# Performance work log

Measured on AMD Instinct MI355X. Metric: run time of the kernel, lower is better.

The kernel has to match this reference:

```python
import jax, jax.numpy as jnp
import numpy as np

B, N, DIM, H, DH = 4, 2048, 1024, 16, 64  # batch, seq, model dim, heads, head dim


def setup_inputs() -> dict:
    key = jax.random.key(0)
    k1, k2, k3 = jax.random.split(key, 3)
    x = jax.random.normal(k1, (B, N, DIM), dtype=jnp.float32)
    w_qkv = jax.random.normal(k2, (DIM, 3 * H * DH), dtype=jnp.float32) * (DIM ** -0.5)
    w_out = jax.random.normal(k3, (H * DH, DIM), dtype=jnp.float32) * ((H * DH) ** -0.5)
    b_out = jnp.zeros((DIM,), dtype=jnp.float32)
    return {"x": x, "w_qkv": w_qkv, "w_out": w_out, "b_out": b_out}


def reference(x, w_qkv, w_out, b_out):
    scale = DH ** -0.5
    qkv = x @ w_qkv                              # [b, n, 3*h*d]
    q, k, v = jnp.split(qkv, 3, axis=-1)
    # 'b n (h d) -> b h n d'
    def to_heads(t):
        return t.reshape(B, N, H, DH).transpose(0, 2, 1, 3)
    q, k, v = to_heads(q), to_heads(k), to_heads(v)
    dots = jnp.einsum('bhid,bhjd->bhij', q, k) * scale   # [b, h, n, n]
    attn = jax.nn.softmax(dots, axis=-1)
    out = jnp.einsum('bhij,bhjd->bhid', attn, v)          # [b, h, n, d]
    out = out.transpose(0, 2, 1, 3).reshape(B, N, H * DH) # 'b h n d -> b n (h d)'
    return out @ w_out + b_out
```

## Files before the change

kernel.cpp:

```cpp
#include <hip/hip_runtime.h>
#include <stdint.h>

#define B_    4
#define N_    2048
#define DIM_  1024
#define H_    16
#define DH_   64
#define BN_   (B_ * N_)
#define QKVN_ (3 * H_ * DH_)

typedef unsigned short u16;
typedef __attribute__((ext_vector_type(8))) __bf16 bf16x8;
typedef __attribute__((ext_vector_type(8))) short  short8;
typedef __attribute__((ext_vector_type(4))) float  f32x4;
typedef __attribute__((ext_vector_type(4))) u16    u16x4;

__device__ inline u16 f2bf(float f) {
    union { float f; uint32_t u; } v; v.f = f;
    uint32_t r = v.u + 0x7fffu + ((v.u >> 16) & 1u);
    return (u16)(r >> 16);
}
__device__ inline float bf2f(u16 u) {
    union { uint32_t u; float f; } v; v.u = ((uint32_t)u) << 16;
    return v.f;
}

__global__ __launch_bounds__(256) void cast_f32_bf16(const float* __restrict__ in,
                                                     u16* __restrict__ out, int n4) {
    int i = blockIdx.x * blockDim.x + threadIdx.x;
    int stride = gridDim.x * blockDim.x;
    for (; i < n4; i += stride) {
        float4 v = reinterpret_cast<const float4*>(in)[i];
        u16x4 o;
        o.x = f2bf(v.x); o.y = f2bf(v.y); o.z = f2bf(v.z); o.w = f2bf(v.w);
        reinterpret_cast<u16x4*>(out)[i] = o;
    }
}

__global__ __launch_bounds__(256) void transpose_cast(const float* __restrict__ in,
                                                      u16* __restrict__ out, int R, int C) {
    int gid = blockIdx.x * blockDim.x + threadIdx.x;
    int total = C * (R / 4);
    if (gid >= total) return;
    int n  = gid % C;
    int k4 = (gid / C) * 4;
    u16x4 o;
    o.x = f2bf(in[(size_t)(k4 + 0) * C + n]);
    o.y = f2bf(in[(size_t)(k4 + 1) * C + n]);
    o.z = f2bf(in[(size_t)(k4 + 2) * C + n]);
    o.w = f2bf(in[(size_t)(k4 + 3) * C + n]);
    *reinterpret_cast<u16x4*>(&out[(size_t)n * R + k4]) = o;
}

template <bool BF16_OUT>
__global__ __launch_bounds__(256) void gemm_bt(const u16* __restrict__ A,
                                               const u16* __restrict__ BT,
                                               void* __restrict__ Cout,
                                               const float* __restrict__ bias,
                                               int M, int Nn, int K) {
    __shared__ u16 As[128][40];
    __shared__ u16 Bs[128][40];

    const int tid  = threadIdx.x;
    const int m0   = blockIdx.y * 128;
    const int n0   = blockIdx.x * 128;
    const int w    = tid >> 6;
    const int lane = tid & 63;
    const int lr   = lane & 15;
    const int lg   = lane >> 4;
    const int wm   = w >> 1;
    const int wn   = w & 1;

    f32x4 acc[4][4] = {};

    const int sr = tid >> 2;
    const int sc = (tid & 3) * 8;
    const u16* Aptr = A  + (size_t)(m0 + sr) * K + sc;
    const u16* Bptr = BT + (size_t)(n0 + sr) * K + sc;

    for (int kt = 0; kt < K; kt += 32) {
        *reinterpret_cast<short8*>(&As[sr][sc])      = *reinterpret_cast<const short8*>(Aptr + kt);
        *reinterpret_cast<short8*>(&As[sr + 64][sc]) = *reinterpret_cast<const short8*>(Aptr + (size_t)64 * K + kt);
        *reinterpret_cast<short8*>(&Bs[sr][sc])      = *reinterpret_cast<const short8*>(Bptr + kt);
        *reinterpret_cast<short8*>(&Bs[sr + 64][sc]) = *reinterpret_cast<const short8*>(Bptr + (size_t)64 * K + kt);
        __syncthreads();

        bf16x8 af[4], bfr[4];
#pragma unroll
        for (int m = 0; m < 4; m++)
            af[m] = *reinterpret_cast<const bf16x8*>(&As[wm * 64 + m * 16 + lr][lg * 8]);
#pragma unroll
        for (int n = 0; n < 4; n++)
            bfr[n] = *reinterpret_cast<const bf16x8*>(&Bs[wn * 64 + n * 16 + lr][lg * 8]);
#pragma unroll
        for (int m = 0; m < 4; m++)
#pragma unroll
            for (int n = 0; n < 4; n++)
                acc[m][n] = __builtin_amdgcn_mfma_f32_16x16x32_bf16(af[m], bfr[n], acc[m][n], 0, 0, 0);
        __syncthreads();
    }

#pragma unroll
    for (int m = 0; m < 4; m++)
#pragma unroll
        for (int n = 0; n < 4; n++) {
            const int row = m0 + wm * 64 + m * 16 + lg * 4;
            const int col = n0 + wn * 64 + n * 16 + lr;
#pragma unroll
            for (int r = 0; r < 4; r++) {
                if (BF16_OUT) {
                    ((u16*)Cout)[(size_t)(row + r) * Nn + col] = f2bf(acc[m][n][r]);
                } else {
                    ((float*)Cout)[(size_t)(row + r) * Nn + col] = acc[m][n][r] + bias[col];
                }
            }
        }
}

__global__ __launch_bounds__(256) void attn_kernel(const u16* __restrict__ qkv,
                                                   u16* __restrict__ out) {
    __shared__ __align__(16) u16      Ks[2][64][40];
    __shared__ __align__(16) uint32_t VT32[64 * 36];
    __shared__ __align__(16) u16      Ps[4][16][72];

    const int tid  = threadIdx.x;
    const int w    = tid >> 6;
    const int lane = tid & 63;
    const int lr   = lane & 15;
    const int lg   = lane >> 4;

    const int bh = blockIdx.y;
    const int b  = bh >> 4;
    const int h  = bh & 15;
    const int rowbase = b * N_;
    const int q0 = blockIdx.x * 64;
    const int qoff = h * DH_;

    bf16x8 qf[2];
    {
        const int qrow = rowbase + q0 + w * 16 + lr;
#pragma unroll
        for (int ks = 0; ks < 2; ks++) {
            short8 raw = *reinterpret_cast<const short8*>(
                &qkv[(size_t)qrow * QKVN_ + qoff + ks * 32 + lg * 8]);
            const u16* ru = reinterpret_cast<const u16*>(&raw);
            union { u16 u[8]; bf16x8 v; } q;
#pragma unroll
            for (int j = 0; j < 8; j++) q.u[j] = f2bf(bf2f(ru[j]) * 0.125f);
            qf[ks] = q.v;
        }
    }

    float mrun = -3e38f, lrun = 0.f;
    f32x4 acc_o[4] = {};

    const u16* kg = qkv + (size_t)rowbase * QKVN_ + DIM_ + qoff;
    const u16* vg = qkv + (size_t)rowbase * QKVN_ + 2 * DIM_ + qoff;

    const int kr = tid >> 2;
    const int kc = (tid & 3) * 8;
    const size_t koff0 = (size_t)kr * QKVN_ + kc;
    const int vp  = tid >> 3;
    const int vsc = (tid & 7) * 8;
    const size_t voff0 = (size_t)(vp * 2) * QKVN_ + vsc;
    const size_t voff1 = voff0 + QKVN_;

    short8 kst[2], vst[2];
    kst[0] = *reinterpret_cast<const short8*>(kg + koff0);
    kst[1] = *reinterpret_cast<const short8*>(kg + koff0 + 32);
    vst[0] = *reinterpret_cast<const short8*>(vg + voff0);
    vst[1] = *reinterpret_cast<const short8*>(vg + voff1);

    *reinterpret_cast<short8*>(&Ks[0][kr][kc]) = kst[0];
    *reinterpret_cast<short8*>(&Ks[1][kr][kc]) = kst[1];
    {
        const u16* v0 = reinterpret_cast<const u16*>(&vst[0]);
        const u16* v1 = reinterpret_cast<const u16*>(&vst[1]);
#pragma unroll
        for (int i = 0; i < 8; i++) {
            const int d = vsc + i;
            const int col = vp ^ (((d >> 2) & 7) << 2);
            VT32[d * 36 + col] = (uint32_t)v0[i] | ((uint32_t)v1[i] << 16);
        }
    }
    __syncthreads();

    for (int t = 0; t < N_ / 64; t++) {
        if (t + 1 < N_ / 64) {
            const u16* kg2 = kg + (size_t)(t + 1) * 64 * QKVN_;
            const u16* vg2 = vg + (size_t)(t + 1) * 64 * QKVN_;
            kst[0] = *reinterpret_cast<const short8*>(kg2 + koff0);
            kst[1] = *reinterpret_cast<const short8*>(kg2 + koff0 + 32);
            vst[0] = *reinterpret_cast<const short8*>(vg2 + voff0);
            vst[1] = *reinterpret_cast<const short8*>(vg2 + voff1);
        }

        f32x4 s[4];
#pragma unroll
        for (int n = 0; n < 4; n++) {
            bf16x8 k0 = *reinterpret_cast<const bf16x8*>(&Ks[0][n * 16 + lr][lg * 8]);
            bf16x8 k1 = *reinterpret_cast<const bf16x8*>(&Ks[1][n * 16 + lr][lg * 8]);
            f32x4 z = {0.f, 0.f, 0.f, 0.f};
            s[n] = __builtin_amdgcn_mfma_f32_16x16x32_bf16(k0, qf[0], z, 0, 0, 0);
            s[n] = __builtin_amdgcn_mfma_f32_16x16x32_bf16(k1, qf[1], s[n], 0, 0, 0);
        }

        float tmax = fmaxf(fmaxf(s[0][0], s[0][1]), fmaxf(s[0][2], s[0][3]));
#pragma unroll
        for (int n = 1; n < 4; n++)
            tmax = fmaxf(tmax, fmaxf(fmaxf(s[n][0], s[n][1]), fmaxf(s[n][2], s[n][3])));
        tmax = fmaxf(tmax, __shfl_xor(tmax, 16));
        tmax = fmaxf(tmax, __shfl_xor(tmax, 32));
        float mnew = fmaxf(mrun, tmax);
        float fac = __expf(mrun - mnew);
        mrun = mnew;
        float psum = 0.f;
#pragma unroll
        for (int n = 0; n < 4; n++) {
            float p0 = __expf(s[n][0] - mnew);
            float p1 = __expf(s[n][1] - mnew);
            float p2 = __expf(s[n][2] - mnew);
            float p3 = __expf(s[n][3] - mnew);
            psum += (p0 + p1) + (p2 + p3);
            u16x4 pw;
            pw.x = f2bf(p0); pw.y = f2bf(p1); pw.z = f2bf(p2); pw.w = f2bf(p3);
            *reinterpret_cast<u16x4*>(&Ps[w][lr][n * 16 + lg * 4]) = pw;
        }
        psum += __shfl_xor(psum, 16);
        psum += __shfl_xor(psum, 32);
        lrun = lrun * fac + psum;

        float facq[4];
#pragma unroll
        for (int r = 0; r < 4; r++) facq[r] = __shfl(fac, (lane & 48) | (lg * 4 + r));
#pragma unroll
        for (int n = 0; n < 4; n++)
#pragma unroll
            for (int r = 0; r < 4; r++) acc_o[n][r] *= facq[r];

#pragma unroll
        for (int c = 0; c < 2; c++) {
            bf16x8 pa = *reinterpret_cast<const bf16x8*>(&Ps[w][lr][c * 32 + lg * 8]);
#pragma unroll
            for (int n = 0; n < 4; n++) {
                const int d = n * 16 + lr;
                const int bc = (c * 16 + lg * 4) ^ (((d >> 2) & 7) << 2);
                bf16x8 vf = *reinterpret_cast<const bf16x8*>(&VT32[d * 36 + bc]);
                acc_o[n] = __builtin_amdgcn_mfma_f32_16x16x32_bf16(pa, vf, acc_o[n], 0, 0, 0);
            }
        }

        __syncthreads();
        if (t + 1 < N_ / 64) {
            *reinterpret_cast<short8*>(&Ks[0][kr][kc]) = kst[0];
            *reinterpret_cast<short8*>(&Ks[1][kr][kc]) = kst[1];
            const u16* v0 = reinterpret_cast<const u16*>(&vst[0]);
            const u16* v1 = reinterpret_cast<const u16*>(&vst[1]);
#pragma unroll
            for (int i = 0; i < 8; i++) {
                const int d = vsc + i;
                const int col = vp ^ (((d >> 2) & 7) << 2);
                VT32[d * 36 + col] = (uint32_t)v0[i] | ((uint32_t)v1[i] << 16);
            }
        }
        __syncthreads();
    }

    float linv = 1.f / lrun;
    float lq[4];
#pragma unroll
    for (int r = 0; r < 4; r++) lq[r] = __shfl(linv, (lane & 48) | (lg * 4 + r));
#pragma unroll
    for (int n = 0; n < 4; n++)
#pragma unroll
        for (int r = 0; r < 4; r++) {
            const int row = rowbase + q0 + w * 16 + lg * 4 + r;
            const int col = qoff + n * 16 + lr;
            out[(size_t)row * DIM_ + col] = f2bf(acc_o[n][r] * lq[r]);
        }
}

extern "C" void kernel_launch(void* const* d_in, const int* in_sizes, int n_in,
                              void* d_out, int out_size, void* d_ws, size_t ws_size,
                              hipStream_t stream) {
    const float* x     = (const float*)d_in[0];
    const float* w_qkv = (const float*)d_in[1];
    const float* w_out = (const float*)d_in[2];
    const float* b_out = (const float*)d_in[3];
    float* out = (float*)d_out;

    char* ws = (char*)d_ws;
    u16* xbf   = (u16*)(ws);
    u16* wqkvT = (u16*)(ws + 16777216);
    u16* woutT = (u16*)(ws + 23068672);
    u16* qkv   = (u16*)(ws + 25165824);
    u16* attnO = (u16*)(ws + 75497472);

    cast_f32_bf16<<<2048, 256, 0, stream>>>(x, xbf, (BN_ * DIM_) / 4);
    transpose_cast<<<(DIM_ / 4) * QKVN_ / 256, 256, 0, stream>>>(w_qkv, wqkvT, DIM_, QKVN_);
    transpose_cast<<<(DIM_ / 4) * DIM_ / 256, 256, 0, stream>>>(w_out, woutT, DIM_, DIM_);

    gemm_bt<true><<<dim3(QKVN_ / 128, BN_ / 128), 256, 0, stream>>>(
        xbf, wqkvT, qkv, nullptr, BN_, QKVN_, DIM_);

    attn_kernel<<<dim3(N_ / 64, B_ * H_), 256, 0, stream>>>(qkv, attnO);

    gemm_bt<false><<<dim3(DIM_ / 128, BN_ / 128), 256, 0, stream>>>(
        attnO, woutT, out, b_out, BN_, DIM_, DIM_);
}
```

Baseline: 363.3 us.

## Use direct global-to-LDS loads, exp2 softmax with lazy rescale, hardware bf16 convert

The GEMM tile load now uses global_load_lds to write straight into unpadded shared memory, skipping the register round trip. The attention kernel folds log2(e) into the Q scale so it can use exp2f. It skips the running-max rescale of the accumulator unless the new max exceeds the old one by more than a threshold. It also precomputes the swizzled V offsets outside the loop and uses the native bf16 conversion instead of manual rounding. The unpadded LDS layout may add bank conflicts on the fragment reads. The lazy rescale keeps the result exact in principle but lets values grow by up to 2^8 before renormalising.

```diff
diff --git a/kernel.cpp b/kernel.cpp
--- a/kernel.cpp
+++ b/kernel.cpp
@@ -9,6 +9,9 @@
 #define BN_   (B_ * N_)
 #define QKVN_ (3 * H_ * DH_)
 
+#define AS1_ __attribute__((address_space(1)))
+#define AS3_ __attribute__((address_space(3)))
+
 typedef unsigned short u16;
 typedef __attribute__((ext_vector_type(8))) __bf16 bf16x8;
 typedef __attribute__((ext_vector_type(8))) short  short8;
@@ -16,9 +19,7 @@
 typedef __attribute__((ext_vector_type(4))) u16    u16x4;
 
 __device__ inline u16 f2bf(float f) {
-    union { float f; uint32_t u; } v; v.f = f;
-    uint32_t r = v.u + 0x7fffu + ((v.u >> 16) & 1u);
-    return (u16)(r >> 16);
+    union { __bf16 b; u16 u; } v; v.b = (__bf16)f; return v.u;
 }
 __device__ inline float bf2f(u16 u) {
     union { uint32_t u; float f; } v; v.u = ((uint32_t)u) << 16;
@@ -58,8 +59,8 @@
                                                void* __restrict__ Cout,
                                                const float* __restrict__ bias,
                                                int M, int Nn, int K) {
-    __shared__ u16 As[128][40];
-    __shared__ u16 Bs[128][40];
+    __shared__ __align__(16) u16 AsF[128 * 32];
+    __shared__ __align__(16) u16 BsF[128 * 32];
 
     const int tid  = threadIdx.x;
     const int m0   = blockIdx.y * 128;
@@ -77,21 +78,26 @@
     const int sc = (tid & 3) * 8;
     const u16* Aptr = A  + (size_t)(m0 + sr) * K + sc;
     const u16* Bptr = BT + (size_t)(n0 + sr) * K + sc;
+    const int ldsb = w * 512;
 
     for (int kt = 0; kt < K; kt += 32) {
-        *reinterpret_cast<short8*>(&As[sr][sc])      = *reinterpret_cast<const short8*>(Aptr + kt);
-        *reinterpret_cast<short8*>(&As[sr + 64][sc]) = *reinterpret_cast<const short8*>(Aptr + (size_t)64 * K + kt);
-        *reinterpret_cast<short8*>(&Bs[sr][sc])      = *reinterpret_cast<const short8*>(Bptr + kt);
-        *reinterpret_cast<short8*>(&Bs[sr + 64][sc]) = *reinterpret_cast<const short8*>(Bptr + (size_t)64 * K + kt);
+        __builtin_amdgcn_global_load_lds((const AS1_ void*)(Aptr + kt),
+                                         (AS3_ void*)&AsF[ldsb], 16, 0, 0);
+        __builtin_amdgcn_global_load_lds((const AS1_ void*)(Aptr + (size_t)64 * K + kt),
+                                         (AS3_ void*)&AsF[2048 + ldsb], 16, 0, 0);
+        __builtin_amdgcn_global_load_lds((const AS1_ void*)(Bptr + kt),
+                                         (AS3_ void*)&BsF[ldsb], 16, 0, 0);
+        __builtin_amdgcn_global_load_lds((const AS1_ void*)(Bptr + (size_t)64 * K + kt),
+                                         (AS3_ void*)&BsF[2048 + ldsb], 16, 0, 0);
         __syncthreads();
 
         bf16x8 af[4], bfr[4];
 #pragma unroll
         for (int m = 0; m < 4; m++)
-            af[m] = *reinterpret_cast<const bf16x8*>(&As[wm * 64 + m * 16 + lr][lg * 8]);
+            af[m] = *reinterpret_cast<const bf16x8*>(&AsF[(wm * 64 + m * 16 + lr) * 32 + lg * 8]);
 #pragma unroll
         for (int n = 0; n < 4; n++)
-            bfr[n] = *reinterpret_cast<const bf16x8*>(&Bs[wn * 64 + n * 16 + lr][lg * 8]);
+            bfr[n] = *reinterpret_cast<const bf16x8*>(&BsF[(wn * 64 + n * 16 + lr) * 32 + lg * 8]);
 #pragma unroll
         for (int m = 0; m < 4; m++)
 #pragma unroll
@@ -138,6 +144,7 @@
 
     bf16x8 qf[2];
     {
+        const float qscale = 0.125f * 1.4426950408889634f;
         const int qrow = rowbase + q0 + w * 16 + lr;
 #pragma unroll
         for (int ks = 0; ks < 2; ks++) {
@@ -146,7 +153,7 @@
             const u16* ru = reinterpret_cast<const u16*>(&raw);
             union { u16 u[8]; bf16x8 v; } q;
 #pragma unroll
-            for (int j = 0; j < 8; j++) q.u[j] = f2bf(bf2f(ru[j]) * 0.125f);
+            for (int j = 0; j < 8; j++) q.u[j] = f2bf(bf2f(ru[j]) * qscale);
             qf[ks] = q.v;
         }
     }
@@ -164,6 +171,15 @@
     const int vsc = (tid & 7) * 8;
     const size_t voff0 = (size_t)(vp * 2) * QKVN_ + vsc;
     const size_t voff1 = voff0 + QKVN_;
+
+    int vb_off[2][4];
+#pragma unroll
+    for (int c = 0; c < 2; c++)
+#pragma unroll
+        for (int n = 0; n < 4; n++) {
+            const int d = n * 16 + lr;
+            vb_off[c][n] = d * 36 + ((c * 16 + lg * 4) ^ (((d >> 2) & 7) << 2));
+        }
 
     short8 kst[2], vst[2];
     kst[0] = *reinterpret_cast<const short8*>(kg + koff0);
@@ -211,16 +227,28 @@
             tmax = fmaxf(tmax, fmaxf(fmaxf(s[n][0], s[n][1]), fmaxf(s[n][2], s[n][3])));
         tmax = fmaxf(tmax, __shfl_xor(tmax, 16));
         tmax = fmaxf(tmax, __shfl_xor(tmax, 32));
-        float mnew = fmaxf(mrun, tmax);
-        float fac = __expf(mrun - mnew);
-        mrun = mnew;
+
+        if (!__all(tmax - mrun <= 8.f)) {
+            float mnew = fmaxf(mrun, tmax);
+            float fac  = exp2f(mrun - mnew);
+            mrun = mnew;
+            lrun *= fac;
+            float facq[4];
+#pragma unroll
+            for (int r = 0; r < 4; r++) facq[r] = __shfl(fac, (lane & 48) | (lg * 4 + r));
+#pragma unroll
+            for (int n = 0; n < 4; n++)
+#pragma unroll
+                for (int r = 0; r < 4; r++) acc_o[n][r] *= facq[r];
+        }
+
         float psum = 0.f;
 #pragma unroll
         for (int n = 0; n < 4; n++) {
-            float p0 = __expf(s[n][0] - mnew);
-            float p1 = __expf(s[n][1] - mnew);
-            float p2 = __expf(s[n][2] - mnew);
-            float p3 = __expf(s[n][3] - mnew);
+            float p0 = exp2f(s[n][0] - mrun);
+            float p1 = exp2f(s[n][1] - mrun);
+            float p2 = exp2f(s[n][2] - mrun);
+            float p3 = exp2f(s[n][3] - mrun);
             psum += (p0 + p1) + (p2 + p3);
             u16x4 pw;
             pw.x = f2bf(p0); pw.y = f2bf(p1); pw.z = f2bf(p2); pw.w = f2bf(p3);
@@ -228,24 +256,14 @@
         }
         psum += __shfl_xor(psum, 16);
         psum += __shfl_xor(psum, 32);
-        lrun = lrun * fac + psum;
-
-        float facq[4];
-#pragma unroll
-        for (int r = 0; r < 4; r++) facq[r] = __shfl(fac, (lane & 48) | (lg * 4 + r));
-#pragma unroll
-        for (int n = 0; n < 4; n++)
-#pragma unroll
-            for (int r = 0; r < 4; r++) acc_o[n][r] *= facq[r];
+        lrun += psum;
 
 #pragma unroll
         for (int c = 0; c < 2; c++) {
             bf16x8 pa = *reinterpret_cast<const bf16x8*>(&Ps[w][lr][c * 32 + lg * 8]);
 #pragma unroll
             for (int n = 0; n < 4; n++) {
-                const int d = n * 16 + lr;
-                const int bc = (c * 16 + lg * 4) ^ (((d >> 2) & 7) << 2);
-                bf16x8 vf = *reinterpret_cast<const bf16x8*>(&VT32[d * 36 + bc]);
+                bf16x8 vf = *reinterpret_cast<const bf16x8*>(&VT32[vb_off[c][n]]);
                 acc_o[n] = __builtin_amdgcn_mfma_f32_16x16x32_bf16(pa, vf, acc_o[n], 0, 0, 0);
             }
         }
```

Result: faster. 351.8 us (-3.2%).
